# Optimization experiments

Hardware: AMD Instinct MI355X
Metric: run time of the kernel (lower is better)

The kernel has to match this reference:

```python
import jax, jax.numpy as jnp
import numpy as np
from jax import lax

R = 14            # resolution (fixed by relative-position bias table)
N = R * R         # 196 tokens
DIM = 384
HEADS = 8
HD = DIM // HEADS
SCALE = HD ** -0.5
B = 128
C3 = DIM * 3


def _bias_idx():
    # identical algorithm to the torch module: discovery-order offset ids
    pts = [(i, j) for i in range(R) for j in range(R)]
    offs = {}
    idxs = []
    for p1 in pts:
        for p2 in pts:
            o = (abs(p1[0] - p2[0]), abs(p1[1] - p2[1]))
            if o not in offs:
                offs[o] = len(offs)
            idxs.append(offs[o])
    return np.asarray(idxs, dtype=np.int32).reshape(N, N), len(offs)


def setup_inputs() -> dict:
    key = jax.random.key(0)
    ks = iter(jax.random.split(key, 48))
    nrm = lambda shape, s=0.02: jax.random.normal(next(ks), shape, jnp.float32) * s
    idx, n_off = _bias_idx()  # n_off == 196 for R=14
    inp = {
        'll': jax.random.normal(next(ks), (B, DIM, R, R), jnp.float32),
        'lh': jax.random.normal(next(ks), (B, DIM, R, R), jnp.float32),
        'hl': jax.random.normal(next(ks), (B, DIM, R, R), jnp.float32),
        'hh': jax.random.normal(next(ks), (B, DIM, R, R), jnp.float32),
        # RepVGGDW (BN folded): depthwise 3x3 + depthwise 1x1 (per-channel scale)
        'dw3_w': nrm((C3, 1, 3, 3), 0.1), 'dw3_b': nrm((C3,)),
        'dw1_w': nrm((C3,), 0.1), 'dw1_b': nrm((C3,)),
        # high_fuse_pw: 3C -> C 1x1 (BN folded)
        'pw_w': nrm((DIM, C3)), 'pw_b': nrm((DIM,)),
        # HighFreqMHSA
        'hqkv_w': nrm((3 * DIM, DIM)), 'hqkv_b': nrm((3 * DIM,)),
        'hproj_w': nrm((DIM, DIM)), 'hproj_b': nrm((DIM,)),
        'hbias': nrm((HEADS, n_off), 0.1),
        # high FFN (hidden = 2*dim)
        'hm1_w': nrm((2 * DIM, DIM)), 'hm1_b': nrm((2 * DIM,)),
        'hm2_w': nrm((DIM, 2 * DIM)), 'hm2_b': nrm((DIM,)),
        # EffectiveSE
        'ese_w': nrm((DIM, DIM)), 'ese_b': nrm((DIM,)),
        # LowFreqCrossAttn
        'lq_w': nrm((DIM, DIM)), 'lq_b': nrm((DIM,)),
        'lkv_w': nrm((2 * DIM, DIM)), 'lkv_b': nrm((2 * DIM,)),
        'lproj_w': nrm((DIM, DIM)), 'lproj_b': nrm((DIM,)),
        'lbias': nrm((HEADS, n_off), 0.1),
        # low FFN
        'lm1_w': nrm((2 * DIM, DIM)), 'lm1_b': nrm((2 * DIM,)),
        'lm2_w': nrm((DIM, 2 * DIM)), 'lm2_b': nrm((DIM,)),
        'bias_idx': jnp.asarray(idx),  # int32 [N, N]
    }
    return inp


def _pw(x, w, b):
    # 1x1 conv == channel GEMM
    return jnp.einsum('oi,bihw->bohw', w, x) + b[None, :, None, None]


def _gelu(x):
    return jax.nn.gelu(x, approximate=False)


def _hsig(x):
    return jnp.clip(x / 6.0 + 0.5, 0.0, 1.0)


def _attn(q, k, v, bias):
    # q,k,v: [B,C,H,W]; bias: [heads,N,N]
    b = q.shape[0]
    qh = q.reshape(b, HEADS, HD, N).transpose(0, 1, 3, 2)  # [B,h,N,d]
    kh = k.reshape(b, HEADS, HD, N)                         # [B,h,d,N]
    vh = v.reshape(b, HEADS, HD, N).transpose(0, 1, 3, 2)  # [B,h,N,d]
    a = jnp.einsum('bhnd,bhdm->bhnm', qh, kh) * SCALE + bias[None]
    a = jax.nn.softmax(a, axis=-1)
    o = jnp.einsum('bhnm,bhmd->bhnd', a, vh)
    return o.transpose(0, 1, 3, 2).reshape(b, DIM, R, R)


def reference(ll, lh, hl, hh, dw3_w, dw3_b, dw1_w, dw1_b, pw_w, pw_b,
              hqkv_w, hqkv_b, hproj_w, hproj_b, hbias, hm1_w, hm1_b,
              hm2_w, hm2_b, ese_w, ese_b, lq_w, lq_b, lkv_w, lkv_b,
              lproj_w, lproj_b, lbias, lm1_w, lm1_b, lm2_w, lm2_b, bias_idx):
    # ---- high-frequency branch ----
    hc_in = jnp.concatenate([lh, hl, hh], axis=1)  # [B,3C,H,W]
    dw3 = lax.conv_general_dilated(hc_in, dw3_w, (1, 1), 'SAME',
                                   feature_group_count=C3,
                                   dimension_numbers=('NCHW', 'OIHW', 'NCHW'))
    dw3 = dw3 + dw3_b[None, :, None, None]
    dw1 = hc_in * dw1_w[None, :, None, None] + dw1_b[None, :, None, None]
    high_dw = _gelu(dw3 + dw1 + hc_in)  # RepVGGDW + GELU
    hc = _pw(high_dw, pw_w, pw_b)       # [B,C,H,W]

    qkv = _pw(hc, hqkv_w, hqkv_b)
    q, k, v = jnp.split(qkv, 3, axis=1)
    high_attn_out = hc + _pw(_attn(q, k, v, hbias[:, bias_idx]), hproj_w, hproj_b)
    refined_high = high_attn_out + _pw(_gelu(_pw(high_attn_out, hm1_w, hm1_b)), hm2_w, hm2_b)

    # ---- low-frequency branch ----
    se = ll * _hsig(_pw(ll.mean((2, 3), keepdims=True), ese_w, ese_b))
    lq = _pw(se, lq_w, lq_b)
    kv = _pw(refined_high, lkv_w, lkv_b)
    lk, lv = jnp.split(kv, 2, axis=1)
    ll_attn = se + _pw(_attn(lq, lk, lv, lbias[:, bias_idx]), lproj_w, lproj_b)
    output = ll_attn + _pw(_gelu(_pw(ll_attn, lm1_w, lm1_b)), lm2_w, lm2_b)
    return output
```

## Files before the change

### kernel.cpp

```cpp
#include <hip/hip_runtime.h>
#include <hip/hip_bf16.h>
#include <math.h>

#define TTOK 25088
#define NTOK 196

typedef __bf16 bf16x8_t __attribute__((ext_vector_type(8)));
typedef float f32x4_t __attribute__((ext_vector_type(4)));
typedef __hip_bfloat16 bf16;

__device__ __forceinline__ void async16(void* lds, const void* g) {
  __builtin_amdgcn_global_load_lds((const __attribute__((address_space(1))) unsigned int*)g,
                                   (__attribute__((address_space(3))) unsigned int*)lds, 16, 0, 0);
}

__device__ __forceinline__ float gelu_f(float x) {
  float u = x * (1.5957691216057308f + 0.07135481627f * x * x);
  return x / (1.0f + __expf(-u));
}

__device__ __forceinline__ bf16x8_t zero_bf16x8() {
  bf16x8_t v;
#pragma unroll
  for (int i = 0; i < 8; i++) v[i] = (__bf16)0.0f;
  return v;
}

template<int K, int EPI>
__global__ __launch_bounds__(256) void gemm_bt(
    const bf16* __restrict__ X, const bf16* __restrict__ W,
    const float* __restrict__ bias, const bf16* __restrict__ res,
    bf16* __restrict__ out, float* __restrict__ outf, int Co)
{
  __shared__ __align__(16) bf16 As[128 * 32];
  __shared__ __align__(16) bf16 Bs[128 * 32];
  const int tid = threadIdx.x;
  const int lane = tid & 63;
  const int wv = tid >> 6;
  const int quad = lane >> 4, l15 = lane & 15;
  const int wm = wv >> 1, wn = wv & 1;
  const int t0 = blockIdx.x * 128;
  const int n0 = blockIdx.y * 128;

  f32x4_t acc[4][4];
#pragma unroll
  for (int i = 0; i < 4; i++)
#pragma unroll
    for (int j = 0; j < 4; j++) {
      acc[i][j][0] = 0.f; acc[i][j][1] = 0.f; acc[i][j][2] = 0.f; acc[i][j][3] = 0.f;
    }

  constexpr int KT = K / 32;
  for (int kk = 0; kk < KT; kk++) {
    if (kk) __syncthreads();
#pragma unroll
    for (int j = 0; j < 2; j++) {
      int ch = j * 256 + tid;
      int row = ch >> 2;
      int colb = (ch & 3) << 4;
      async16((char*)As + ch * 16,
              (const char*)X + ((size_t)(t0 + row) * K + kk * 32) * 2 + colb);
      async16((char*)Bs + ch * 16,
              (const char*)W + ((size_t)(n0 + row) * K + kk * 32) * 2 + colb);
    }
    __syncthreads();
    bf16x8_t a[4], b[4];
#pragma unroll
    for (int mt = 0; mt < 4; mt++)
      a[mt] = *(const bf16x8_t*)(As + (wm * 64 + mt * 16 + l15) * 32 + quad * 8);
#pragma unroll
    for (int nt = 0; nt < 4; nt++)
      b[nt] = *(const bf16x8_t*)(Bs + (wn * 64 + nt * 16 + l15) * 32 + quad * 8);
#pragma unroll
    for (int mt = 0; mt < 4; mt++)
#pragma unroll
      for (int nt = 0; nt < 4; nt++)
        acc[mt][nt] = __builtin_amdgcn_mfma_f32_16x16x32_bf16(a[mt], b[nt], acc[mt][nt], 0, 0, 0);
  }

#pragma unroll
  for (int nt = 0; nt < 4; nt++) {
    int co = n0 + wn * 64 + nt * 16 + l15;
    float bv = bias[co];
#pragma unroll
    for (int mt = 0; mt < 4; mt++) {
#pragma unroll
      for (int r = 0; r < 4; r++) {
        int t = t0 + wm * 64 + mt * 16 + quad * 4 + r;
        float v = acc[mt][nt][r] + bv;
        if constexpr (EPI == 1) v = gelu_f(v);
        if constexpr (EPI >= 2) v += (float)res[(size_t)t * Co + co];
        if constexpr (EPI == 3) {
          int bb = t / NTOK, nsp = t % NTOK;
          outf[((size_t)bb * 384 + co) * NTOK + nsp] = v;
        } else {
          out[(size_t)t * Co + co] = bf16(v);
        }
      }
    }
  }
}

__global__ __launch_bounds__(256) void attn_kernel(
    const bf16* __restrict__ q, int sq,
    const bf16* __restrict__ kv, int skv, int kofs0, int vofs0,
    const float* __restrict__ bmat, bf16* __restrict__ outp)
{
  __shared__ __align__(16) bf16 Ks[196 * 48];
  __shared__ __align__(16) bf16 VT[48 * 208];
  __shared__ __align__(16) bf16 Pl[4 * 16 * 208];
  const int b = blockIdx.x >> 3, h = blockIdx.x & 7;
  const int tid = threadIdx.x;
  const int lane = tid & 63, wv = tid >> 6;
  const int quad = lane >> 4, l15 = lane & 15;
  const int qoff = h * 48, koff = kofs0 + h * 48, voff = vofs0 + h * 48;
  const float SC = 0.14433756729740643f;

  for (int j = 0; j < 5; j++) {
    int idx = j * 256 + tid;
    if (idx < 1176) {
      int o = idx * 16;
      int row = o / 96, colb = o % 96;
      async16((char*)Ks + o,
              (const char*)kv + ((size_t)(b * 196 + row) * skv + koff) * 2 + colb);
    }
  }
  for (int i = tid; i < 196 * 48; i += 256) {
    int mk = i / 48, d = i % 48;
    VT[d * 208 + mk] = kv[(size_t)(b * 196 + mk) * skv + voff + d];
  }
  for (int i = tid; i < 48 * 12; i += 256) {
    int d = i / 12, mk = 196 + (i % 12);
    VT[d * 208 + mk] = bf16(0.0f);
  }
  __syncthreads();

  bf16* Pw = Pl + wv * 16 * 208;

  for (int qt = wv; qt < 13; qt += 4) {
    int trow = qt * 16 + l15;
    int tl = trow < 196 ? trow : 195;
    const bf16* qrow = q + (size_t)(b * 196 + tl) * sq + qoff;
    bf16x8_t aq0 = *(const bf16x8_t*)(qrow + quad * 8);
    bf16x8_t aq1 = zero_bf16x8();
    if (quad < 2) aq1 = *(const bf16x8_t*)(qrow + 32 + quad * 8);

    f32x4_t S[13];
#pragma unroll
    for (int kt = 0; kt < 13; kt++) { S[kt][0] = 0.f; S[kt][1] = 0.f; S[kt][2] = 0.f; S[kt][3] = 0.f; }

#pragma unroll
    for (int kt = 0; kt < 13; kt++) {
      int kr = kt * 16 + l15;
      bf16x8_t bk0 = zero_bf16x8(), bk1 = zero_bf16x8();
      if (kr < 196) {
        const bf16* krow = Ks + kr * 48;
        bk0 = *(const bf16x8_t*)(krow + quad * 8);
        if (quad < 2) bk1 = *(const bf16x8_t*)(krow + 32 + quad * 8);
      }
      S[kt] = __builtin_amdgcn_mfma_f32_16x16x32_bf16(aq0, bk0, S[kt], 0, 0, 0);
      S[kt] = __builtin_amdgcn_mfma_f32_16x16x32_bf16(aq1, bk1, S[kt], 0, 0, 0);
    }

    float mrow[4] = {-1e30f, -1e30f, -1e30f, -1e30f};
#pragma unroll
    for (int kt = 0; kt < 13; kt++) {
      int m = kt * 16 + l15;
      int mc = m < 196 ? m : 195;
#pragma unroll
      for (int r = 0; r < 4; r++) {
        int qg = qt * 16 + quad * 4 + r;
        int qc = qg < 196 ? qg : 195;
        float s = S[kt][r] * SC + bmat[((size_t)h * 196 + qc) * 196 + mc];
        if (m >= 196) s = -1e30f;
        S[kt][r] = s;
        mrow[r] = fmaxf(mrow[r], s);
      }
    }
#pragma unroll
    for (int r = 0; r < 4; r++)
#pragma unroll
      for (int off = 1; off < 16; off <<= 1)
        mrow[r] = fmaxf(mrow[r], __shfl_xor(mrow[r], off));
    float srow[4] = {0.f, 0.f, 0.f, 0.f};
#pragma unroll
    for (int kt = 0; kt < 13; kt++)
#pragma unroll
      for (int r = 0; r < 4; r++) {
        float p = __expf(S[kt][r] - mrow[r]);
        S[kt][r] = p;
        srow[r] += p;
      }
#pragma unroll
    for (int r = 0; r < 4; r++) {
#pragma unroll
      for (int off = 1; off < 16; off <<= 1)
        srow[r] += __shfl_xor(srow[r], off);
      srow[r] = 1.0f / srow[r];
    }
#pragma unroll
    for (int kt = 0; kt < 13; kt++)
#pragma unroll
      for (int r = 0; r < 4; r++)
        Pw[(quad * 4 + r) * 208 + kt * 16 + l15] = bf16(S[kt][r] * srow[r]);

    f32x4_t O[3];
#pragma unroll
    for (int dt = 0; dt < 3; dt++) { O[dt][0] = 0.f; O[dt][1] = 0.f; O[dt][2] = 0.f; O[dt][3] = 0.f; }
#pragma unroll
    for (int ks = 0; ks < 7; ks++) {
      bool act = (ks < 6) || (quad < 2);
      bf16x8_t ap = zero_bf16x8();
      if (act) ap = *(const bf16x8_t*)(Pw + l15 * 208 + ks * 32 + quad * 8);
#pragma unroll
      for (int dt = 0; dt < 3; dt++) {
        bf16x8_t bv8 = zero_bf16x8();
        if (act) bv8 = *(const bf16x8_t*)(VT + (dt * 16 + l15) * 208 + ks * 32 + quad * 8);
        O[dt] = __builtin_amdgcn_mfma_f32_16x16x32_bf16(ap, bv8, O[dt], 0, 0, 0);
      }
    }
#pragma unroll
    for (int dt = 0; dt < 3; dt++)
#pragma unroll
      for (int r = 0; r < 4; r++) {
        int tq = qt * 16 + quad * 4 + r;
        if (tq < 196)
          outp[(size_t)(b * 196 + tq) * 384 + qoff + dt * 16 + l15] = bf16(O[dt][r]);
      }
  }
}

__global__ __launch_bounds__(256) void conv_kernel(
    const float* __restrict__ lh, const float* __restrict__ hl, const float* __restrict__ hh,
    const float* __restrict__ w3, const float* __restrict__ b3,
    const float* __restrict__ w1, const float* __restrict__ b1,
    bf16* __restrict__ outp)
{
  __shared__ float plane[64][197];
  const int b = blockIdx.x / 18, chunk = blockIdx.x % 18;
  const int c0 = chunk * 64;
  const float* src = (c0 < 384) ? lh : (c0 < 768 ? hl : hh);
  const int cc0 = c0 % 384;
  for (int i = threadIdx.x; i < 64 * 196; i += 256) {
    int c = i / 196, n = i % 196;
    plane[c][n] = src[((size_t)b * 384 + cc0 + c) * 196 + n];
  }
  __syncthreads();
  const int c = threadIdx.x & 63;
  const int cg = c0 + c;
  float w9[9];
#pragma unroll
  for (int k = 0; k < 9; k++) w9[k] = w3[cg * 9 + k];
  const float bb3 = b3[cg], ww1 = w1[cg], bb1 = b1[cg];

  for (int r = threadIdx.x >> 6; r < 14; r += 4) {
    float rm[14], rc[14], rp[14];
#pragma unroll
    for (int w = 0; w < 14; w++) rc[w] = plane[c][r * 14 + w];
    if (r > 0) {
#pragma unroll
      for (int w = 0; w < 14; w++) rm[w] = plane[c][(r - 1) * 14 + w];
    } else {
#pragma unroll
      for (int w = 0; w < 14; w++) rm[w] = 0.f;
    }
    if (r < 13) {
#pragma unroll
      for (int w = 0; w < 14; w++) rp[w] = plane[c][(r + 1) * 14 + w];
    } else {
#pragma unroll
      for (int w = 0; w < 14; w++) rp[w] = 0.f;
    }
#pragma unroll
    for (int w = 0; w < 14; w++) {
      float s = bb3;
      if (w > 0)  s += rm[w - 1] * w9[0] + rc[w - 1] * w9[3] + rp[w - 1] * w9[6];
      s += rm[w] * w9[1] + rc[w] * w9[4] + rp[w] * w9[7];
      if (w < 13) s += rm[w + 1] * w9[2] + rc[w + 1] * w9[5] + rp[w + 1] * w9[8];
      float x = rc[w];
      float tot = s + x * ww1 + bb1 + x;
      outp[((size_t)b * 196 + r * 14 + w) * 1152 + cg] = bf16(gelu_f(tot));
    }
  }
}

__global__ __launch_bounds__(256) void pool_kernel(
    const float* __restrict__ ll, float* __restrict__ pooled)
{
  const int b = blockIdx.x / 6, chunk = blockIdx.x % 6;
  const int c0 = chunk * 64;
  const int wv = threadIdx.x >> 6, lane = threadIdx.x & 63;
  for (int c = wv; c < 64; c += 4) {
    const float* p = ll + ((size_t)b * 384 + c0 + c) * 196;
    float v = p[lane] + p[64 + lane] + p[128 + lane] + (lane < 4 ? p[192 + lane] : 0.f);
#pragma unroll
    for (int off = 32; off; off >>= 1) v += __shfl_xor(v, off);
    if (lane == 0) pooled[b * 384 + c0 + c] = v * (1.0f / 196.0f);
  }
}

__global__ __launch_bounds__(384) void sescale_kernel(
    const float* __restrict__ pooled, const float* __restrict__ ew,
    const float* __restrict__ eb, float* __restrict__ scale)
{
  __shared__ float pl[384];
  const int b = blockIdx.x;
  const int c = threadIdx.x;
  pl[c] = pooled[b * 384 + c];
  __syncthreads();
  float acc = eb[c];
  const float* wr = ew + (size_t)c * 384;
#pragma unroll 8
  for (int k = 0; k < 384; k++) acc += wr[k] * pl[k];
  float y = acc * (1.0f / 6.0f) + 0.5f;
  scale[b * 384 + c] = fminf(fmaxf(y, 0.f), 1.f);
}

__global__ __launch_bounds__(256) void seapply_kernel(
    const float* __restrict__ ll, const float* __restrict__ scale,
    bf16* __restrict__ se)
{
  __shared__ float plane[64][197];
  const int b = blockIdx.x / 6, chunk = blockIdx.x % 6;
  const int c0 = chunk * 64;
  for (int i = threadIdx.x; i < 64 * 196; i += 256) {
    int c = i / 196, n = i % 196;
    plane[c][n] = ll[((size_t)b * 384 + c0 + c) * 196 + n];
  }
  __syncthreads();
  const int c = threadIdx.x & 63;
  const float sc = scale[b * 384 + c0 + c];
  for (int n = threadIdx.x >> 6; n < 196; n += 4)
    se[((size_t)b * 196 + n) * 384 + c0 + c] = bf16(plane[c][n] * sc);
}

__global__ __launch_bounds__(256) void wconvert_kernel(
    const float* p0, const float* p1, const float* p2, const float* p3, const float* p4,
    const float* p5, const float* p6, const float* p7, const float* p8, const float* p9,
    bf16* dst)
{
  int i = blockIdx.x * 256 + threadIdx.x;
  if (i >= 2801664) return;
  const int offs[11] = {0, 442368, 884736, 1032192, 1327104, 1622016,
                        1769472, 2064384, 2211840, 2506752, 2801664};
  const float* ps[10] = {p0, p1, p2, p3, p4, p5, p6, p7, p8, p9};
  int seg = 0;
#pragma unroll
  for (int k = 1; k < 10; k++) if (i >= offs[k]) seg = k;
  dst[i] = bf16(ps[seg][i - offs[seg]]);
}

__global__ __launch_bounds__(256) void biasmat_kernel(
    const float* __restrict__ hbias, const float* __restrict__ lbias,
    const int* __restrict__ idx, float* __restrict__ bh, float* __restrict__ bl)
{
  int i = blockIdx.x * 256 + threadIdx.x;
  if (i >= 307328) return;
  int h = i / 38416;
  int nm = i % 38416;
  int id = idx[nm];
  bh[i] = hbias[h * 196 + id];
  bl[i] = lbias[h * 196 + id];
}

extern "C" void kernel_launch(void* const* d_in, const int* in_sizes, int n_in,
                              void* d_out, int out_size, void* d_ws, size_t ws_size,
                              hipStream_t stream) {
  const float* ll     = (const float*)d_in[0];
  const float* lh     = (const float*)d_in[1];
  const float* hl     = (const float*)d_in[2];
  const float* hh     = (const float*)d_in[3];
  const float* dw3_w  = (const float*)d_in[4];
  const float* dw3_b  = (const float*)d_in[5];
  const float* dw1_w  = (const float*)d_in[6];
  const float* dw1_b  = (const float*)d_in[7];
  const float* pw_w   = (const float*)d_in[8];
  const float* pw_b   = (const float*)d_in[9];
  const float* hqkv_w = (const float*)d_in[10];
  const float* hqkv_b = (const float*)d_in[11];
  const float* hproj_w= (const float*)d_in[12];
  const float* hproj_b= (const float*)d_in[13];
  const float* hbias  = (const float*)d_in[14];
  const float* hm1_w  = (const float*)d_in[15];
  const float* hm1_b  = (const float*)d_in[16];
  const float* hm2_w  = (const float*)d_in[17];
  const float* hm2_b  = (const float*)d_in[18];
  const float* ese_w  = (const float*)d_in[19];
  const float* ese_b  = (const float*)d_in[20];
  const float* lq_w   = (const float*)d_in[21];
  const float* lq_b   = (const float*)d_in[22];
  const float* lkv_w  = (const float*)d_in[23];
  const float* lkv_b  = (const float*)d_in[24];
  const float* lproj_w= (const float*)d_in[25];
  const float* lproj_b= (const float*)d_in[26];
  const float* lbias  = (const float*)d_in[27];
  const float* lm1_w  = (const float*)d_in[28];
  const float* lm1_b  = (const float*)d_in[29];
  const float* lm2_w  = (const float*)d_in[30];
  const float* lm2_b  = (const float*)d_in[31];
  const int* bias_idx = (const int*)d_in[32];

  char* ws = (char*)d_ws;
  bf16*  WB = (bf16*)(ws);
  float* BH = (float*)(ws + 5603328);
  float* BL = (float*)(ws + 6832640);
  bf16*  A  = (bf16*)(ws + 8061952);
  bf16*  B1 = (bf16*)(ws + 65864704);
  bf16*  B2 = (bf16*)(ws + 85132288);
  bf16*  B3 = (bf16*)(ws + 104399872);
  bf16*  B4 = (bf16*)(ws + 123667456);
  bf16*  E  = (bf16*)(ws + 162202624);
  float* PO = (float*)(ws + 181470208);
  float* SC = (float*)(ws + 181666816);
  float* OUT = (float*)d_out;

  wconvert_kernel<<<10945, 256, 0, stream>>>(pw_w, hqkv_w, hproj_w, hm1_w, hm2_w,
                                             lq_w, lkv_w, lproj_w, lm1_w, lm2_w, WB);
  biasmat_kernel<<<1201, 256, 0, stream>>>(hbias, lbias, bias_idx, BH, BL);
  conv_kernel<<<2304, 256, 0, stream>>>(lh, hl, hh, dw3_w, dw3_b, dw1_w, dw1_b, A);
  pool_kernel<<<768, 256, 0, stream>>>(ll, PO);
  sescale_kernel<<<128, 384, 0, stream>>>(PO, ese_w, ese_b, SC);
  seapply_kernel<<<768, 256, 0, stream>>>(ll, SC, E);

  gemm_bt<1152, 0><<<dim3(196, 3), 256, 0, stream>>>(A, WB + 0, pw_b, nullptr, B1, nullptr, 384);
  gemm_bt<384, 0><<<dim3(196, 9), 256, 0, stream>>>(B1, WB + 442368, hqkv_b, nullptr, A, nullptr, 1152);
  attn_kernel<<<1024, 256, 0, stream>>>(A, 1152, A, 1152, 384, 768, BH, B2);
  gemm_bt<384, 2><<<dim3(196, 3), 256, 0, stream>>>(B2, WB + 884736, hproj_b, B1, B3, nullptr, 384);
  gemm_bt<384, 1><<<dim3(196, 6), 256, 0, stream>>>(B3, WB + 1032192, hm1_b, nullptr, B4, nullptr, 768);
  gemm_bt<768, 2><<<dim3(196, 3), 256, 0, stream>>>(B4, WB + 1327104, hm2_b, B3, B1, nullptr, 384);

  gemm_bt<384, 0><<<dim3(196, 6), 256, 0, stream>>>(B1, WB + 1769472, lkv_b, nullptr, B4, nullptr, 768);
  gemm_bt<384, 0><<<dim3(196, 3), 256, 0, stream>>>(E, WB + 1622016, lq_b, nullptr, B2, nullptr, 384);
  attn_kernel<<<1024, 256, 0, stream>>>(B2, 384, B4, 768, 0, 384, BL, B1);
  gemm_bt<384, 2><<<dim3(196, 3), 256, 0, stream>>>(B1, WB + 2064384, lproj_b, E, B3, nullptr, 384);
  gemm_bt<384, 1><<<dim3(196, 6), 256, 0, stream>>>(B3, WB + 2211840, lm1_b, nullptr, A, nullptr, 768);
  gemm_bt<768, 3><<<dim3(196, 3), 256, 0, stream>>>(A, WB + 2506752, lm2_b, B3, nullptr, OUT, 384);
}
```

Measured before the change: 793.8 us.

## Add 64-row GEMM tiles, restructure depthwise conv, fuse SE scale into apply

The GEMM kernel is templated on the M tile, and the 384-output-channel GEMMs launch with 64-row tiles and 128 threads. This doubles the block count so the narrow GEMMs fill more of the GPU. The depthwise conv now stores its input plane in bf16 LDS, folds the 1x1 and identity terms into the centre tap, and computes two output rows per thread from four loaded rows. The SE excitation matvec is merged into the apply kernel with wave reductions, which removes one launch. The risks are extra bf16 rounding of the conv input and lower per-block reuse in the small-tile GEMMs.

```diff
diff --git a/kernel.cpp b/kernel.cpp
--- a/kernel.cpp
+++ b/kernel.cpp
@@ -1,6 +1,7 @@
 #include <hip/hip_runtime.h>
 #include <hip/hip_bf16.h>
 #include <math.h>
+#include <stdint.h>
 
 #define TTOK 25088
 #define NTOK 196
@@ -19,6 +20,9 @@
   return x / (1.0f + __expf(-u));
 }
 
+__device__ __forceinline__ float lo_bf(uint32_t u) { return __uint_as_float(u << 16); }
+__device__ __forceinline__ float hi_bf(uint32_t u) { return __uint_as_float(u & 0xffff0000u); }
+
 __device__ __forceinline__ bf16x8_t zero_bf16x8() {
   bf16x8_t v;
 #pragma unroll
@@ -26,20 +30,22 @@
   return v;
 }
 
-template<int K, int EPI>
-__global__ __launch_bounds__(256) void gemm_bt(
+template<int K, int EPI, int MT>
+__global__ __launch_bounds__(MT * 2) void gemm_bt(
     const bf16* __restrict__ X, const bf16* __restrict__ W,
     const float* __restrict__ bias, const bf16* __restrict__ res,
     bf16* __restrict__ out, float* __restrict__ outf, int Co)
 {
-  __shared__ __align__(16) bf16 As[128 * 32];
+  __shared__ __align__(16) bf16 As[MT * 32];
   __shared__ __align__(16) bf16 Bs[128 * 32];
+  constexpr int T = MT * 2;
   const int tid = threadIdx.x;
   const int lane = tid & 63;
   const int wv = tid >> 6;
   const int quad = lane >> 4, l15 = lane & 15;
-  const int wm = wv >> 1, wn = wv & 1;
-  const int t0 = blockIdx.x * 128;
+  const int wm = (MT == 128) ? (wv >> 1) : 0;
+  const int wn = (MT == 128) ? (wv & 1) : wv;
+  const int t0 = blockIdx.x * MT;
   const int n0 = blockIdx.y * 128;
 
   f32x4_t acc[4][4];
@@ -54,12 +60,16 @@
   for (int kk = 0; kk < KT; kk++) {
     if (kk) __syncthreads();
 #pragma unroll
-    for (int j = 0; j < 2; j++) {
-      int ch = j * 256 + tid;
+    for (int ch = tid; ch < MT * 4; ch += T) {
       int row = ch >> 2;
       int colb = (ch & 3) << 4;
       async16((char*)As + ch * 16,
               (const char*)X + ((size_t)(t0 + row) * K + kk * 32) * 2 + colb);
+    }
+#pragma unroll
+    for (int ch = tid; ch < 512; ch += T) {
+      int row = ch >> 2;
+      int colb = (ch & 3) << 4;
       async16((char*)Bs + ch * 16,
               (const char*)W + ((size_t)(n0 + row) * K + kk * 32) * 2 + colb);
     }
@@ -230,56 +240,67 @@
   }
 }
 
-__global__ __launch_bounds__(256) void conv_kernel(
+__global__ __launch_bounds__(256, 4) void conv_kernel(
     const float* __restrict__ lh, const float* __restrict__ hl, const float* __restrict__ hh,
     const float* __restrict__ w3, const float* __restrict__ b3,
     const float* __restrict__ w1, const float* __restrict__ b1,
     bf16* __restrict__ outp)
 {
-  __shared__ float plane[64][197];
+  __shared__ bf16 plane[64 * 198];
+  const int tid = threadIdx.x;
   const int b = blockIdx.x / 18, chunk = blockIdx.x % 18;
   const int c0 = chunk * 64;
   const float* src = (c0 < 384) ? lh : (c0 < 768 ? hl : hh);
   const int cc0 = c0 % 384;
-  for (int i = threadIdx.x; i < 64 * 196; i += 256) {
-    int c = i / 196, n = i % 196;
-    plane[c][n] = src[((size_t)b * 384 + cc0 + c) * 196 + n];
+#pragma unroll 7
+  for (int k = 0; k < 49; k++) {
+    int idx = k * 256 + tid;
+    int c = idx / 196, n = idx % 196;
+    plane[c * 198 + n] = bf16(src[((size_t)b * 384 + cc0 + c) * 196 + n]);
   }
   __syncthreads();
-  const int c = threadIdx.x & 63;
+  const int c = tid & 63;
   const int cg = c0 + c;
   float w9[9];
 #pragma unroll
   for (int k = 0; k < 9; k++) w9[k] = w3[cg * 9 + k];
-  const float bb3 = b3[cg], ww1 = w1[cg], bb1 = b1[cg];
-
-  for (int r = threadIdx.x >> 6; r < 14; r += 4) {
-    float rm[14], rc[14], rp[14];
-#pragma unroll
-    for (int w = 0; w < 14; w++) rc[w] = plane[c][r * 14 + w];
-    if (r > 0) {
-#pragma unroll
-      for (int w = 0; w < 14; w++) rm[w] = plane[c][(r - 1) * 14 + w];
-    } else {
-#pragma unroll
-      for (int w = 0; w < 14; w++) rm[w] = 0.f;
-    }
-    if (r < 13) {
-#pragma unroll
-      for (int w = 0; w < 14; w++) rp[w] = plane[c][(r + 1) * 14 + w];
-    } else {
-#pragma unroll
-      for (int w = 0; w < 14; w++) rp[w] = 0.f;
-    }
-#pragma unroll
-    for (int w = 0; w < 14; w++) {
-      float s = bb3;
-      if (w > 0)  s += rm[w - 1] * w9[0] + rc[w - 1] * w9[3] + rp[w - 1] * w9[6];
-      s += rm[w] * w9[1] + rc[w] * w9[4] + rp[w] * w9[7];
-      if (w < 13) s += rm[w + 1] * w9[2] + rc[w + 1] * w9[5] + rp[w + 1] * w9[8];
-      float x = rc[w];
-      float tot = s + x * ww1 + bb1 + x;
-      outp[((size_t)b * 196 + r * 14 + w) * 1152 + cg] = bf16(gelu_f(tot));
+  w9[4] += w1[cg] + 1.0f;
+  const float bb = b3[cg] + b1[cg];
+  const int g = tid >> 6;
+
+  for (int half = 0; half < 2; half++) {
+    int r0 = half * 8 + 2 * g;
+    if (r0 >= 14) break;
+    float rw[4][14];
+#pragma unroll
+    for (int rr = 0; rr < 4; rr++) {
+      int r = r0 - 1 + rr;
+      if (r >= 0 && r < 14) {
+        const uint32_t* prow = (const uint32_t*)(plane + (c * 198 + r * 14));
+#pragma unroll
+        for (int j = 0; j < 7; j++) {
+          uint32_t u = prow[j];
+          rw[rr][2 * j] = lo_bf(u);
+          rw[rr][2 * j + 1] = hi_bf(u);
+        }
+      } else {
+#pragma unroll
+        for (int w = 0; w < 14; w++) rw[rr][w] = 0.f;
+      }
+    }
+#pragma unroll
+    for (int rr = 0; rr < 2; rr++) {
+      int r = r0 + rr;
+      const float* rm = rw[rr];
+      const float* rc = rw[rr + 1];
+      const float* rp = rw[rr + 2];
+#pragma unroll
+      for (int w = 0; w < 14; w++) {
+        float s = bb + rm[w] * w9[1] + rc[w] * w9[4] + rp[w] * w9[7];
+        if (w > 0)  s += rm[w - 1] * w9[0] + rc[w - 1] * w9[3] + rp[w - 1] * w9[6];
+        if (w < 13) s += rm[w + 1] * w9[2] + rc[w + 1] * w9[5] + rp[w + 1] * w9[8];
+        outp[((size_t)b * 196 + r * 14 + w) * 1152 + cg] = bf16(gelu_f(s));
+      }
     }
   }
 }
@@ -299,38 +320,41 @@
   }
 }
 
-__global__ __launch_bounds__(384) void sescale_kernel(
-    const float* __restrict__ pooled, const float* __restrict__ ew,
-    const float* __restrict__ eb, float* __restrict__ scale)
+__global__ __launch_bounds__(256) void seapply_kernel(
+    const float* __restrict__ ll, const float* __restrict__ pooled,
+    const float* __restrict__ ew, const float* __restrict__ eb,
+    bf16* __restrict__ se)
 {
   __shared__ float pl[384];
-  const int b = blockIdx.x;
-  const int c = threadIdx.x;
-  pl[c] = pooled[b * 384 + c];
-  __syncthreads();
-  float acc = eb[c];
-  const float* wr = ew + (size_t)c * 384;
-#pragma unroll 8
-  for (int k = 0; k < 384; k++) acc += wr[k] * pl[k];
-  float y = acc * (1.0f / 6.0f) + 0.5f;
-  scale[b * 384 + c] = fminf(fmaxf(y, 0.f), 1.f);
-}
-
-__global__ __launch_bounds__(256) void seapply_kernel(
-    const float* __restrict__ ll, const float* __restrict__ scale,
-    bf16* __restrict__ se)
-{
+  __shared__ float scale[64];
   __shared__ float plane[64][197];
+  const int tid = threadIdx.x;
   const int b = blockIdx.x / 6, chunk = blockIdx.x % 6;
   const int c0 = chunk * 64;
-  for (int i = threadIdx.x; i < 64 * 196; i += 256) {
+  const int wv = tid >> 6, lane = tid & 63;
+
+  for (int i = tid; i < 384; i += 256) pl[i] = pooled[b * 384 + i];
+  for (int i = tid; i < 64 * 196; i += 256) {
     int c = i / 196, n = i % 196;
     plane[c][n] = ll[((size_t)b * 384 + c0 + c) * 196 + n];
   }
   __syncthreads();
-  const int c = threadIdx.x & 63;
-  const float sc = scale[b * 384 + c0 + c];
-  for (int n = threadIdx.x >> 6; n < 196; n += 4)
+  for (int cc = wv; cc < 64; cc += 4) {
+    const float* wr = ew + (size_t)(c0 + cc) * 384;
+    float v = 0.f;
+#pragma unroll
+    for (int j = 0; j < 6; j++) v += wr[j * 64 + lane] * pl[j * 64 + lane];
+#pragma unroll
+    for (int off = 32; off; off >>= 1) v += __shfl_xor(v, off);
+    if (lane == 0) {
+      float y = (v + eb[c0 + cc]) * (1.0f / 6.0f) + 0.5f;
+      scale[cc] = fminf(fmaxf(y, 0.f), 1.f);
+    }
+  }
+  __syncthreads();
+  const int c = tid & 63;
+  const float sc = scale[c];
+  for (int n = tid >> 6; n < 196; n += 4)
     se[((size_t)b * 196 + n) * 384 + c0 + c] = bf16(plane[c][n] * sc);
 }
 
@@ -411,7 +435,6 @@
   bf16*  B4 = (bf16*)(ws + 123667456);
   bf16*  E  = (bf16*)(ws + 162202624);
   float* PO = (float*)(ws + 181470208);
-  float* SC = (float*)(ws + 181666816);
   float* OUT = (float*)d_out;
 
   wconvert_kernel<<<10945, 256, 0, stream>>>(pw_w, hqkv_w, hproj_w, hm1_w, hm2_w,
@@ -419,20 +442,19 @@
   biasmat_kernel<<<1201, 256, 0, stream>>>(hbias, lbias, bias_idx, BH, BL);
   conv_kernel<<<2304, 256, 0, stream>>>(lh, hl, hh, dw3_w, dw3_b, dw1_w, dw1_b, A);
   pool_kernel<<<768, 256, 0, stream>>>(ll, PO);
-  sescale_kernel<<<128, 384, 0, stream>>>(PO, ese_w, ese_b, SC);
-  seapply_kernel<<<768, 256, 0, stream>>>(ll, SC, E);
-
-  gemm_bt<1152, 0><<<dim3(196, 3), 256, 0, stream>>>(A, WB + 0, pw_b, nullptr, B1, nullptr, 384);
-  gemm_bt<384, 0><<<dim3(196, 9), 256, 0, stream>>>(B1, WB + 442368, hqkv_b, nullptr, A, nullptr, 1152);
+  seapply_kernel<<<768, 256, 0, stream>>>(ll, PO, ese_w, ese_b, E);
+
+  gemm_bt<1152, 0, 64><<<dim3(392, 3), 128, 0, stream>>>(A, WB + 0, pw_b, nullptr, B1, nullptr, 384);
+  gemm_bt<384, 0, 128><<<dim3(196, 9), 256, 0, stream>>>(B1, WB + 442368, hqkv_b, nullptr, A, nullptr, 1152);
   attn_kernel<<<1024, 256, 0, stream>>>(A, 1152, A, 1152, 384, 768, BH, B2);
-  gemm_bt<384, 2><<<dim3(196, 3), 256, 0, stream>>>(B2, WB + 884736, hproj_b, B1, B3, nullptr, 384);
-  gemm_bt<384, 1><<<dim3(196, 6), 256, 0, stream>>>(B3, WB + 1032192, hm1_b, nullptr, B4, nullptr, 768);
-  gemm_bt<768, 2><<<dim3(196, 3), 256, 0, stream>>>(B4, WB + 1327104, hm2_b, B3, B1, nullptr, 384);
-
-  gemm_bt<384, 0><<<dim3(196, 6), 256, 0, stream>>>(B1, WB + 1769472, lkv_b, nullptr, B4, nullptr, 768);
-  gemm_bt<384, 0><<<dim3(196, 3), 256, 0, stream>>>(E, WB + 1622016, lq_b, nullptr, B2, nullptr, 384);
+  gemm_bt<384, 2, 64><<<dim3(392, 3), 128, 0, stream>>>(B2, WB + 884736, hproj_b, B1, B3, nullptr, 384);
+  gemm_bt<384, 1, 128><<<dim3(196, 6), 256, 0, stream>>>(B3, WB + 1032192, hm1_b, nullptr, B4, nullptr, 768);
+  gemm_bt<768, 2, 64><<<dim3(392, 3), 128, 0, stream>>>(B4, WB + 1327104, hm2_b, B3, B1, nullptr, 384);
+
+  gemm_bt<384, 0, 128><<<dim3(196, 6), 256, 0, stream>>>(B1, WB + 1769472, lkv_b, nullptr, B4, nullptr, 768);
+  gemm_bt<384, 0, 64><<<dim3(392, 3), 128, 0, stream>>>(E, WB + 1622016, lq_b, nullptr, B2, nullptr, 384);
   attn_kernel<<<1024, 256, 0, stream>>>(B2, 384, B4, 768, 0, 384, BL, B1);
-  gemm_bt<384, 2><<<dim3(196, 3), 256, 0, stream>>>(B1, WB + 2064384, lproj_b, E, B3, nullptr, 384);
-  gemm_bt<384, 1><<<dim3(196, 6), 256, 0, stream>>>(B3, WB + 2211840, lm1_b, nullptr, A, nullptr, 768);
-  gemm_bt<768, 3><<<dim3(196, 3), 256, 0, stream>>>(A, WB + 2506752, lm2_b, B3, nullptr, OUT, 384);
-}
+  gemm_bt<384, 2, 64><<<dim3(392, 3), 128, 0, stream>>>(B1, WB + 2064384, lproj_b, E, B3, nullptr, 384);
+  gemm_bt<384, 1, 128><<<dim3(196, 6), 256, 0, stream>>>(B3, WB + 2211840, lm1_b, nullptr, A, nullptr, 768);
+  gemm_bt<768, 3, 64><<<dim3(392, 3), 128, 0, stream>>>(A, WB + 2506752, lm2_b, B3, nullptr, OUT, 384);
+}
```

Measured after the change: 779.0 us. About the same (-1.9%).
